# Optimization experiments

Hardware: AMD Instinct MI355X
Metric: run time of the kernel (lower is better)

## Reference

```python
import jax, jax.numpy as jnp
import numpy as np

# Geometry / discretization constants (mirrors WaveCell.__init__)
NX, NY = 192, 192
DT = 1e-3
CMAX = 1.0
H = DT * CMAX * np.sqrt(2.0) * 1.01  # auto-set h as in __init__ (satisfies CFL)
SRC_X, SRC_Y = 96, 32  # point source grid location


def _laplacian(y, inv_h2):
    # y: [B, Nx, Ny]; 5-point stencil with zero padding (conv2d padding=1)
    p = jnp.pad(y, ((0, 0), (1, 1), (1, 1)))
    return inv_h2 * (p[:, :-2, 1:-1] + p[:, 2:, 1:-1]
                     + p[:, 1:-1, :-2] + p[:, 1:-1, 2:] - 4.0 * y)


def setup_inputs() -> dict:
    key = jax.random.key(0)
    k1, k2, k3 = jax.random.split(key, 3)
    B, T = 4, 256
    x = jax.random.normal(k1, (B, T, 1), dtype=jnp.float32)
    # per-cell wave speed in [0,1) so cmax <= 1 (CFL-safe)
    c = jax.random.uniform(k2, (NX, NY), dtype=jnp.float32)
    # boundary absorber damping coefficient
    b = jax.random.uniform(k3, (NX, NY), dtype=jnp.float32)
    return {"x": x, "c": c, "b": b}


def reference(x, c, b):
    B, T = x.shape[0], x.shape[1]
    inv_h2 = 1.0 / (H * H)
    inv_dt2 = 1.0 / (DT * DT)
    a_inv = 1.0 / (inv_dt2 + 0.5 * b / DT)   # [Nx, Ny]
    coef2 = inv_dt2 - 0.5 * b / DT           # [Nx, Ny]
    c2 = c * c

    x_seq = jnp.transpose(x[..., 0], (1, 0))  # [T, B]

    def step(carry, xt):
        y1, y2 = carry  # fields one and two steps ago
        y = a_inv * (2.0 * inv_dt2 * y1 - coef2 * y2 + c2 * _laplacian(y1, inv_h2))
        y = y.at[:, SRC_X, SRC_Y].add(xt)  # point source injection
        return (y, y1), y

    y0 = jnp.zeros((B, NX, NY), dtype=x.dtype)
    _, ys = jax.lax.scan(step, (y0, y0), x_seq)  # ys: [T, B, Nx, Ny]
    return jnp.transpose(ys, (1, 0, 2, 3))       # [B, T, Nx, Ny]
```

## Files before the change

### kernel.cpp

```cpp
#include <hip/hip_runtime.h>


#define NXg 192
#define NYg 192
#define BATCH 4
#define TSTEPS 256
#define CELLS (NXg * NYg)

#define TS 24
#define KSTEP 16
#define EXT 56
#define LROWS (EXT + 2)
#define LPITCH 68
#define LSZ (LROWS * LPITCH)
#define NTHREADS 448

#define SRC_X 96
#define SRC_Y 32

__global__ __launch_bounds__(NTHREADS) void wave_tile_kernel(
    const float* __restrict__ cgp, const float* __restrict__ bgp,
    const float* __restrict__ x, float* __restrict__ out, int t0) {
  __shared__ float buf0[LSZ];
  __shared__ float buf1[LSZ];

  const int tid = threadIdx.x;
  const int lr = tid >> 3;
  const int lg = tid & 7;
  const int bcol = blockIdx.x;
  const int brow = blockIdx.y;
  const int bb = blockIdx.z;
  const int r0 = brow * TS - KSTEP;
  const int c0 = bcol * TS - KSTEP;
  const int obase = bb * TSTEPS * CELLS;
  const float inv_h2 = (float)(1.0 / (2.0 * 1.01 * 1.01 * 1.0e-3 * 1.0e-3));

  const int gr = r0 + lr;
  const int gc = c0 + 8 * lg;
  const bool id = (lg < 7) && (gr >= 0) && (gr < NXg) && (gc >= 0) && (gc < NYg);
  const bool til = (lr >= KSTEP) && (lr < KSTEP + TS) && (lg >= 2) && (lg < 5);
  const bool hs = (SRC_X >= r0) && (SRC_X < r0 + EXT) &&
                  (SRC_Y >= c0) && (SRC_Y < c0 + EXT);
  const int gofs = id ? (gr * NYg + gc) : 0;

  const float4 z4 = make_float4(0.f, 0.f, 0.f, 0.f);

  float4 cv0 = z4, cv1 = z4, bv0 = z4, bv1 = z4;
  float4 yc0 = z4, yc1 = z4, yp0 = z4, yp1 = z4;
  if (id) {
    cv0 = *(const float4*)(cgp + gofs);
    cv1 = *(const float4*)(cgp + gofs + 4);
    bv0 = *(const float4*)(bgp + gofs);
    bv1 = *(const float4*)(bgp + gofs + 4);
    if (t0 > 0) {
      yc0 = *(const float4*)(out + obase + (t0 - 1) * CELLS + gofs);
      yc1 = *(const float4*)(out + obase + (t0 - 1) * CELLS + gofs + 4);
      yp0 = *(const float4*)(out + obase + (t0 - 2) * CELLS + gofs);
      yp1 = *(const float4*)(out + obase + (t0 - 2) * CELLS + gofs + 4);
    }
  }
  float xs[KSTEP];
  {
    const float4* xp = (const float4*)(x + bb * TSTEPS + t0);
    float4 a0 = xp[0], a1 = xp[1], a2 = xp[2], a3 = xp[3];
    xs[0] = a0.x; xs[1] = a0.y; xs[2] = a0.z; xs[3] = a0.w;
    xs[4] = a1.x; xs[5] = a1.y; xs[6] = a1.z; xs[7] = a1.w;
    xs[8] = a2.x; xs[9] = a2.y; xs[10] = a2.z; xs[11] = a2.w;
    xs[12] = a3.x; xs[13] = a3.y; xs[14] = a3.z; xs[15] = a3.w;
  }

  float4 Dc0 = z4, Dc1 = z4, Ey0 = z4, Ey1 = z4, G0 = z4, G1 = z4;
  float4 sm0 = z4, sm1 = z4;
  if (id) {
    float ai;
    ai = 1.0f / (1.0e6f + 500.0f * bv0.x);
    Dc0.x = 2.0e6f * ai; Ey0.x = (1.0e6f - 500.0f * bv0.x) * ai;
    G0.x = (cv0.x * cv0.x) * inv_h2 * ai;
    ai = 1.0f / (1.0e6f + 500.0f * bv0.y);
    Dc0.y = 2.0e6f * ai; Ey0.y = (1.0e6f - 500.0f * bv0.y) * ai;
    G0.y = (cv0.y * cv0.y) * inv_h2 * ai;
    ai = 1.0f / (1.0e6f + 500.0f * bv0.z);
    Dc0.z = 2.0e6f * ai; Ey0.z = (1.0e6f - 500.0f * bv0.z) * ai;
    G0.z = (cv0.z * cv0.z) * inv_h2 * ai;
    ai = 1.0f / (1.0e6f + 500.0f * bv0.w);
    Dc0.w = 2.0e6f * ai; Ey0.w = (1.0e6f - 500.0f * bv0.w) * ai;
    G0.w = (cv0.w * cv0.w) * inv_h2 * ai;
    ai = 1.0f / (1.0e6f + 500.0f * bv1.x);
    Dc1.x = 2.0e6f * ai; Ey1.x = (1.0e6f - 500.0f * bv1.x) * ai;
    G1.x = (cv1.x * cv1.x) * inv_h2 * ai;
    ai = 1.0f / (1.0e6f + 500.0f * bv1.y);
    Dc1.y = 2.0e6f * ai; Ey1.y = (1.0e6f - 500.0f * bv1.y) * ai;
    G1.y = (cv1.y * cv1.y) * inv_h2 * ai;
    ai = 1.0f / (1.0e6f + 500.0f * bv1.z);
    Dc1.z = 2.0e6f * ai; Ey1.z = (1.0e6f - 500.0f * bv1.z) * ai;
    G1.z = (cv1.z * cv1.z) * inv_h2 * ai;
    ai = 1.0f / (1.0e6f + 500.0f * bv1.w);
    Dc1.w = 2.0e6f * ai; Ey1.w = (1.0e6f - 500.0f * bv1.w) * ai;
    G1.w = (cv1.w * cv1.w) * inv_h2 * ai;
    if (gr == SRC_X) {
      sm0.x = (gc + 0 == SRC_Y) ? 1.0f : 0.0f;
      sm0.y = (gc + 1 == SRC_Y) ? 1.0f : 0.0f;
      sm0.z = (gc + 2 == SRC_Y) ? 1.0f : 0.0f;
      sm0.w = (gc + 3 == SRC_Y) ? 1.0f : 0.0f;
      sm1.x = (gc + 4 == SRC_Y) ? 1.0f : 0.0f;
      sm1.y = (gc + 5 == SRC_Y) ? 1.0f : 0.0f;
      sm1.z = (gc + 6 == SRC_Y) ? 1.0f : 0.0f;
      sm1.w = (gc + 7 == SRC_Y) ? 1.0f : 0.0f;
    }
  }

  const int lo = (lr + 1) * LPITCH + 4 + 8 * lg;
  *(float4*)&buf0[lo] = yc0;
  *(float4*)&buf0[lo + 4] = yc1;
  __syncthreads();

  float* ping = buf0;
  float* pong = buf1;

  float4 pv0 = z4, pv1 = z4;
  float* pop = out;

#define CELL(dst, up_, dn_, lf_, rt_, D_, E_, Gc_, y_, p_)              \
  {                                                                     \
    float s_ = fmaf(-4.0f, y_, (up_ + dn_) + (lf_ + rt_));              \
    dst = fmaf(Gc_, s_, fmaf(-E_, p_, D_ * y_));                        \
  }

#pragma unroll
  for (int j = 0; j < KSTEP; ++j) {
    const float xt = xs[j];
    float* op = out + obase + (t0 + j) * CELLS;

    if (j > 0 && til) {
      *(float4*)(pop + gofs) = pv0;
      *(float4*)(pop + gofs + 4) = pv1;
    }

    const bool alive = (lr >= j + 1) && (lr <= 54 - j);
    if (alive) {
      float lqw = __shfl_up(yc1.w, 1);
      lqw = (lg == 0) ? 0.0f : lqw;
      float rqx = __shfl_down(yc0.x, 1);
      rqx = (lg == 7) ? 0.0f : rqx;

      float4 up0 = *(float4*)&ping[lo - LPITCH];
      float4 up1 = *(float4*)&ping[lo - LPITCH + 4];
      float4 dn0 = *(float4*)&ping[lo + LPITCH];
      float4 dn1 = *(float4*)&ping[lo + LPITCH + 4];

      float4 val0, val1;
      CELL(val0.x, up0.x, dn0.x, lqw,    yc0.y, Dc0.x, Ey0.x, G0.x, yc0.x, yp0.x);
      CELL(val0.y, up0.y, dn0.y, yc0.x,  yc0.z, Dc0.y, Ey0.y, G0.y, yc0.y, yp0.y);
      CELL(val0.z, up0.z, dn0.z, yc0.y,  yc0.w, Dc0.z, Ey0.z, G0.z, yc0.z, yp0.z);
      CELL(val0.w, up0.w, dn0.w, yc0.z,  yc1.x, Dc0.w, Ey0.w, G0.w, yc0.w, yp0.w);
      CELL(val1.x, up1.x, dn1.x, yc0.w,  yc1.y, Dc1.x, Ey1.x, G1.x, yc1.x, yp1.x);
      CELL(val1.y, up1.y, dn1.y, yc1.x,  yc1.z, Dc1.y, Ey1.y, G1.y, yc1.y, yp1.y);
      CELL(val1.z, up1.z, dn1.z, yc1.y,  yc1.w, Dc1.z, Ey1.z, G1.z, yc1.z, yp1.z);
      CELL(val1.w, up1.w, dn1.w, yc1.z,  rqx,   Dc1.w, Ey1.w, G1.w, yc1.w, yp1.w);

      if (hs) {
        val0.x = fmaf(sm0.x, xt, val0.x);
        val0.y = fmaf(sm0.y, xt, val0.y);
        val0.z = fmaf(sm0.z, xt, val0.z);
        val0.w = fmaf(sm0.w, xt, val0.w);
        val1.x = fmaf(sm1.x, xt, val1.x);
        val1.y = fmaf(sm1.y, xt, val1.y);
        val1.z = fmaf(sm1.z, xt, val1.z);
        val1.w = fmaf(sm1.w, xt, val1.w);
      }

      yp0 = yc0; yp1 = yc1;
      yc0 = val0; yc1 = val1;

      *(float4*)&pong[lo] = val0;
      *(float4*)&pong[lo + 4] = val1;

      pv0 = val0; pv1 = val1;
    }
    pop = op;

    __syncthreads();
    float* tmp = ping; ping = pong; pong = tmp;
  }
#undef CELL

  if (til) {
    *(float4*)(pop + gofs) = pv0;
    *(float4*)(pop + gofs + 4) = pv1;
  }
}

extern "C" void kernel_launch(void* const* d_in, const int* in_sizes, int n_in,
                              void* d_out, int out_size, void* d_ws,
                              size_t ws_size, hipStream_t stream) {
  const float* x = (const float*)d_in[0];
  const float* c = (const float*)d_in[1];
  const float* b = (const float*)d_in[2];
  float* out = (float*)d_out;

  dim3 grid(NXg / TS, NYg / TS, BATCH);
  for (int t0 = 0; t0 < TSTEPS; t0 += KSTEP) {
    wave_tile_kernel<<<grid, NTHREADS, 0, stream>>>(c, b, x, out, t0);
  }
}
```

Before: 324.2 us.

## Run each tile in a single wavefront with register slots, dropping block barriers

Each tile is now handled by one 64-lane wavefront in which every thread owns 7 row slots, replacing the 448-thread block. This removes __syncthreads between time steps, relying on a single wave plus an lgkmcnt wait for LDS ordering. The per-step live-row trimming is dropped, so every slot computes every step, and the update is refactored to y + E*(y-p) + G*lap to save a multiply. The costs are far fewer waves in flight (256 single-wave blocks), heavy register pressure, and serialised work per wave, which may hurt latency hiding.

```diff
diff --git a/kernel.cpp b/kernel.cpp
--- a/kernel.cpp
+++ b/kernel.cpp
@@ -10,23 +10,30 @@
 #define TS 24
 #define KSTEP 16
 #define EXT 56
-#define LROWS (EXT + 2)
+#define LROWS 58
 #define LPITCH 68
 #define LSZ (LROWS * LPITCH)
-#define NTHREADS 448
+#define NSLOT 7
 
 #define SRC_X 96
 #define SRC_Y 32
 
-__global__ __launch_bounds__(NTHREADS) void wave_tile_kernel(
+#define CELL(dst, up_, dn_, lf_, rt_, E_, G_, y_, p_)                  \
+  {                                                                    \
+    float s_ = fmaf(-4.0f, y_, (up_ + dn_) + (lf_ + rt_));             \
+    dst = fmaf(G_, s_, fmaf(E_, (y_ - p_), y_));                       \
+  }
+
+__global__ __launch_bounds__(64, 1) void wave_kernel(
     const float* __restrict__ cgp, const float* __restrict__ bgp,
     const float* __restrict__ x, float* __restrict__ out, int t0) {
   __shared__ float buf0[LSZ];
   __shared__ float buf1[LSZ];
-
-  const int tid = threadIdx.x;
-  const int lr = tid >> 3;
-  const int lg = tid & 7;
+  __shared__ float xsL[KSTEP];
+
+  const int lane = threadIdx.x;
+  const int rs = lane >> 3;
+  const int lg = lane & 7;
   const int bcol = blockIdx.x;
   const int brow = blockIdx.y;
   const int bb = blockIdx.z;
@@ -35,158 +42,151 @@
   const int obase = bb * TSTEPS * CELLS;
   const float inv_h2 = (float)(1.0 / (2.0 * 1.01 * 1.01 * 1.0e-3 * 1.0e-3));
 
-  const int gr = r0 + lr;
   const int gc = c0 + 8 * lg;
-  const bool id = (lg < 7) && (gr >= 0) && (gr < NXg) && (gc >= 0) && (gc < NYg);
-  const bool til = (lr >= KSTEP) && (lr < KSTEP + TS) && (lg >= 2) && (lg < 5);
+  const bool colOK = (lg < 7) && (gc >= 0) && (gc < NYg);
   const bool hs = (SRC_X >= r0) && (SRC_X < r0 + EXT) &&
                   (SRC_Y >= c0) && (SRC_Y < c0 + EXT);
-  const int gofs = id ? (gr * NYg + gc) : 0;
 
   const float4 z4 = make_float4(0.f, 0.f, 0.f, 0.f);
 
-  float4 cv0 = z4, cv1 = z4, bv0 = z4, bv1 = z4;
-  float4 yc0 = z4, yc1 = z4, yp0 = z4, yp1 = z4;
-  if (id) {
-    cv0 = *(const float4*)(cgp + gofs);
-    cv1 = *(const float4*)(cgp + gofs + 4);
-    bv0 = *(const float4*)(bgp + gofs);
-    bv1 = *(const float4*)(bgp + gofs + 4);
-    if (t0 > 0) {
-      yc0 = *(const float4*)(out + obase + (t0 - 1) * CELLS + gofs);
-      yc1 = *(const float4*)(out + obase + (t0 - 1) * CELLS + gofs + 4);
-      yp0 = *(const float4*)(out + obase + (t0 - 2) * CELLS + gofs);
-      yp1 = *(const float4*)(out + obase + (t0 - 2) * CELLS + gofs + 4);
+  float4 smc0 = z4, smc1 = z4;
+  if (colOK) {
+    smc0.x = (gc + 0 == SRC_Y) ? 1.0f : 0.0f;
+    smc0.y = (gc + 1 == SRC_Y) ? 1.0f : 0.0f;
+    smc0.z = (gc + 2 == SRC_Y) ? 1.0f : 0.0f;
+    smc0.w = (gc + 3 == SRC_Y) ? 1.0f : 0.0f;
+    smc1.x = (gc + 4 == SRC_Y) ? 1.0f : 0.0f;
+    smc1.y = (gc + 5 == SRC_Y) ? 1.0f : 0.0f;
+    smc1.z = (gc + 6 == SRC_Y) ? 1.0f : 0.0f;
+    smc1.w = (gc + 7 == SRC_Y) ? 1.0f : 0.0f;
+  }
+
+  int offs[NSLOT];
+  int gofs[NSLOT];
+  bool idv[NSLOT];
+  bool tils[NSLOT];
+  float fs[NSLOT];
+  float4 E[NSLOT][2], G[NSLOT][2];
+  float4 yc[NSLOT][2], yp[NSLOT][2];
+
+#pragma unroll
+  for (int s = 0; s < NSLOT; ++s) {
+    const int lr = rs + 8 * s;
+    const int gr = r0 + lr;
+    const bool idr = colOK && (gr >= 0) && (gr < NXg);
+    idv[s] = idr;
+    gofs[s] = idr ? (gr * NYg + gc) : 0;
+    offs[s] = (lr + 1) * LPITCH + 4 + 8 * lg;
+    tils[s] = (s >= 2) && (s <= 4) && (lg >= 2) && (lg < 5);
+    fs[s] = (gr == SRC_X) ? 1.0f : 0.0f;
+    E[s][0] = z4; E[s][1] = z4; G[s][0] = z4; G[s][1] = z4;
+    yc[s][0] = z4; yc[s][1] = z4; yp[s][0] = z4; yp[s][1] = z4;
+    if (idr) {
+      float4 cv0 = *(const float4*)(cgp + gofs[s]);
+      float4 cv1 = *(const float4*)(cgp + gofs[s] + 4);
+      float4 bv0 = *(const float4*)(bgp + gofs[s]);
+      float4 bv1 = *(const float4*)(bgp + gofs[s] + 4);
+      float ai;
+      ai = 1.0f / (1.0e6f + 500.0f * bv0.x);
+      E[s][0].x = (1.0e6f - 500.0f * bv0.x) * ai; G[s][0].x = cv0.x * cv0.x * inv_h2 * ai;
+      ai = 1.0f / (1.0e6f + 500.0f * bv0.y);
+      E[s][0].y = (1.0e6f - 500.0f * bv0.y) * ai; G[s][0].y = cv0.y * cv0.y * inv_h2 * ai;
+      ai = 1.0f / (1.0e6f + 500.0f * bv0.z);
+      E[s][0].z = (1.0e6f - 500.0f * bv0.z) * ai; G[s][0].z = cv0.z * cv0.z * inv_h2 * ai;
+      ai = 1.0f / (1.0e6f + 500.0f * bv0.w);
+      E[s][0].w = (1.0e6f - 500.0f * bv0.w) * ai; G[s][0].w = cv0.w * cv0.w * inv_h2 * ai;
+      ai = 1.0f / (1.0e6f + 500.0f * bv1.x);
+      E[s][1].x = (1.0e6f - 500.0f * bv1.x) * ai; G[s][1].x = cv1.x * cv1.x * inv_h2 * ai;
+      ai = 1.0f / (1.0e6f + 500.0f * bv1.y);
+      E[s][1].y = (1.0e6f - 500.0f * bv1.y) * ai; G[s][1].y = cv1.y * cv1.y * inv_h2 * ai;
+      ai = 1.0f / (1.0e6f + 500.0f * bv1.z);
+      E[s][1].z = (1.0e6f - 500.0f * bv1.z) * ai; G[s][1].z = cv1.z * cv1.z * inv_h2 * ai;
+      ai = 1.0f / (1.0e6f + 500.0f * bv1.w);
+      E[s][1].w = (1.0e6f - 500.0f * bv1.w) * ai; G[s][1].w = cv1.w * cv1.w * inv_h2 * ai;
+      if (t0 > 0) {
+        const float* o1 = out + obase + (t0 - 1) * CELLS;
+        const float* o2 = out + obase + (t0 - 2) * CELLS;
+        yc[s][0] = *(const float4*)(o1 + gofs[s]);
+        yc[s][1] = *(const float4*)(o1 + gofs[s] + 4);
+        yp[s][0] = *(const float4*)(o2 + gofs[s]);
+        yp[s][1] = *(const float4*)(o2 + gofs[s] + 4);
+      }
     }
   }
-  float xs[KSTEP];
-  {
-    const float4* xp = (const float4*)(x + bb * TSTEPS + t0);
-    float4 a0 = xp[0], a1 = xp[1], a2 = xp[2], a3 = xp[3];
-    xs[0] = a0.x; xs[1] = a0.y; xs[2] = a0.z; xs[3] = a0.w;
-    xs[4] = a1.x; xs[5] = a1.y; xs[6] = a1.z; xs[7] = a1.w;
-    xs[8] = a2.x; xs[9] = a2.y; xs[10] = a2.z; xs[11] = a2.w;
-    xs[12] = a3.x; xs[13] = a3.y; xs[14] = a3.z; xs[15] = a3.w;
-  }
-
-  float4 Dc0 = z4, Dc1 = z4, Ey0 = z4, Ey1 = z4, G0 = z4, G1 = z4;
-  float4 sm0 = z4, sm1 = z4;
-  if (id) {
-    float ai;
-    ai = 1.0f / (1.0e6f + 500.0f * bv0.x);
-    Dc0.x = 2.0e6f * ai; Ey0.x = (1.0e6f - 500.0f * bv0.x) * ai;
-    G0.x = (cv0.x * cv0.x) * inv_h2 * ai;
-    ai = 1.0f / (1.0e6f + 500.0f * bv0.y);
-    Dc0.y = 2.0e6f * ai; Ey0.y = (1.0e6f - 500.0f * bv0.y) * ai;
-    G0.y = (cv0.y * cv0.y) * inv_h2 * ai;
-    ai = 1.0f / (1.0e6f + 500.0f * bv0.z);
-    Dc0.z = 2.0e6f * ai; Ey0.z = (1.0e6f - 500.0f * bv0.z) * ai;
-    G0.z = (cv0.z * cv0.z) * inv_h2 * ai;
-    ai = 1.0f / (1.0e6f + 500.0f * bv0.w);
-    Dc0.w = 2.0e6f * ai; Ey0.w = (1.0e6f - 500.0f * bv0.w) * ai;
-    G0.w = (cv0.w * cv0.w) * inv_h2 * ai;
-    ai = 1.0f / (1.0e6f + 500.0f * bv1.x);
-    Dc1.x = 2.0e6f * ai; Ey1.x = (1.0e6f - 500.0f * bv1.x) * ai;
-    G1.x = (cv1.x * cv1.x) * inv_h2 * ai;
-    ai = 1.0f / (1.0e6f + 500.0f * bv1.y);
-    Dc1.y = 2.0e6f * ai; Ey1.y = (1.0e6f - 500.0f * bv1.y) * ai;
-    G1.y = (cv1.y * cv1.y) * inv_h2 * ai;
-    ai = 1.0f / (1.0e6f + 500.0f * bv1.z);
-    Dc1.z = 2.0e6f * ai; Ey1.z = (1.0e6f - 500.0f * bv1.z) * ai;
-    G1.z = (cv1.z * cv1.z) * inv_h2 * ai;
-    ai = 1.0f / (1.0e6f + 500.0f * bv1.w);
-    Dc1.w = 2.0e6f * ai; Ey1.w = (1.0e6f - 500.0f * bv1.w) * ai;
-    G1.w = (cv1.w * cv1.w) * inv_h2 * ai;
-    if (gr == SRC_X) {
-      sm0.x = (gc + 0 == SRC_Y) ? 1.0f : 0.0f;
-      sm0.y = (gc + 1 == SRC_Y) ? 1.0f : 0.0f;
-      sm0.z = (gc + 2 == SRC_Y) ? 1.0f : 0.0f;
-      sm0.w = (gc + 3 == SRC_Y) ? 1.0f : 0.0f;
-      sm1.x = (gc + 4 == SRC_Y) ? 1.0f : 0.0f;
-      sm1.y = (gc + 5 == SRC_Y) ? 1.0f : 0.0f;
-      sm1.z = (gc + 6 == SRC_Y) ? 1.0f : 0.0f;
-      sm1.w = (gc + 7 == SRC_Y) ? 1.0f : 0.0f;
-    }
-  }
-
-  const int lo = (lr + 1) * LPITCH + 4 + 8 * lg;
-  *(float4*)&buf0[lo] = yc0;
-  *(float4*)&buf0[lo + 4] = yc1;
-  __syncthreads();
+
+  if (lane < 4) {
+    float4 a = ((const float4*)(x + bb * TSTEPS + t0))[lane];
+    *(float4*)&xsL[4 * lane] = a;
+  }
+
+  for (int i = lane; i < 2 * LPITCH; i += 64) {
+    const int row = (i < LPITCH) ? 0 : (LROWS - 1);
+    const int cidx = i % LPITCH;
+    buf0[row * LPITCH + cidx] = 0.f;
+    buf1[row * LPITCH + cidx] = 0.f;
+  }
+
+#pragma unroll
+  for (int s = 0; s < NSLOT; ++s) {
+    *(float4*)&buf0[offs[s]] = yc[s][0];
+    *(float4*)&buf0[offs[s] + 4] = yc[s][1];
+  }
 
   float* ping = buf0;
   float* pong = buf1;
 
-  float4 pv0 = z4, pv1 = z4;
-  float* pop = out;
-
-#define CELL(dst, up_, dn_, lf_, rt_, D_, E_, Gc_, y_, p_)              \
-  {                                                                     \
-    float s_ = fmaf(-4.0f, y_, (up_ + dn_) + (lf_ + rt_));              \
-    dst = fmaf(Gc_, s_, fmaf(-E_, p_, D_ * y_));                        \
-  }
+#pragma clang loop unroll(disable)
+  for (int j = 0; j < KSTEP; ++j) {
+    asm volatile("s_waitcnt lgkmcnt(0)" ::: "memory");
+    const float xt = xsL[j];
+    float* op = out + obase + (t0 + j) * CELLS;
 
 #pragma unroll
-  for (int j = 0; j < KSTEP; ++j) {
-    const float xt = xs[j];
-    float* op = out + obase + (t0 + j) * CELLS;
-
-    if (j > 0 && til) {
-      *(float4*)(pop + gofs) = pv0;
-      *(float4*)(pop + gofs + 4) = pv1;
+    for (int s = 0; s < NSLOT; ++s) {
+      float4 up0 = *(float4*)&ping[offs[s] - LPITCH];
+      float4 up1 = *(float4*)&ping[offs[s] - LPITCH + 4];
+      float4 dn0 = *(float4*)&ping[offs[s] + LPITCH];
+      float4 dn1 = *(float4*)&ping[offs[s] + LPITCH + 4];
+
+      float lq = __shfl_up(yc[s][1].w, 1);
+      lq = (lg == 0) ? 0.0f : lq;
+      float rq = __shfl_down(yc[s][0].x, 1);
+      rq = (lg == 7) ? 0.0f : rq;
+
+      float4 v0, v1;
+      CELL(v0.x, up0.x, dn0.x, lq,         yc[s][0].y, E[s][0].x, G[s][0].x, yc[s][0].x, yp[s][0].x);
+      CELL(v0.y, up0.y, dn0.y, yc[s][0].x, yc[s][0].z, E[s][0].y, G[s][0].y, yc[s][0].y, yp[s][0].y);
+      CELL(v0.z, up0.z, dn0.z, yc[s][0].y, yc[s][0].w, E[s][0].z, G[s][0].z, yc[s][0].z, yp[s][0].z);
+      CELL(v0.w, up0.w, dn0.w, yc[s][0].z, yc[s][1].x, E[s][0].w, G[s][0].w, yc[s][0].w, yp[s][0].w);
+      CELL(v1.x, up1.x, dn1.x, yc[s][0].w, yc[s][1].y, E[s][1].x, G[s][1].x, yc[s][1].x, yp[s][1].x);
+      CELL(v1.y, up1.y, dn1.y, yc[s][1].x, yc[s][1].z, E[s][1].y, G[s][1].y, yc[s][1].y, yp[s][1].y);
+      CELL(v1.z, up1.z, dn1.z, yc[s][1].y, yc[s][1].w, E[s][1].z, G[s][1].z, yc[s][1].z, yp[s][1].z);
+      CELL(v1.w, up1.w, dn1.w, yc[s][1].z, rq,         E[s][1].w, G[s][1].w, yc[s][1].w, yp[s][1].w);
+
+      if (hs) {
+        const float fx = fs[s] * xt;
+        v0.x = fmaf(smc0.x, fx, v0.x);
+        v0.y = fmaf(smc0.y, fx, v0.y);
+        v0.z = fmaf(smc0.z, fx, v0.z);
+        v0.w = fmaf(smc0.w, fx, v0.w);
+        v1.x = fmaf(smc1.x, fx, v1.x);
+        v1.y = fmaf(smc1.y, fx, v1.y);
+        v1.z = fmaf(smc1.z, fx, v1.z);
+        v1.w = fmaf(smc1.w, fx, v1.w);
+      }
+
+      if (tils[s]) {
+        *(float4*)(op + gofs[s]) = v0;
+        *(float4*)(op + gofs[s] + 4) = v1;
+      }
+
+      *(float4*)&pong[offs[s]] = v0;
+      *(float4*)&pong[offs[s] + 4] = v1;
+      yp[s][0] = yc[s][0]; yp[s][1] = yc[s][1];
+      yc[s][0] = v0;       yc[s][1] = v1;
     }
 
-    const bool alive = (lr >= j + 1) && (lr <= 54 - j);
-    if (alive) {
-      float lqw = __shfl_up(yc1.w, 1);
-      lqw = (lg == 0) ? 0.0f : lqw;
-      float rqx = __shfl_down(yc0.x, 1);
-      rqx = (lg == 7) ? 0.0f : rqx;
-
-      float4 up0 = *(float4*)&ping[lo - LPITCH];
-      float4 up1 = *(float4*)&ping[lo - LPITCH + 4];
-      float4 dn0 = *(float4*)&ping[lo + LPITCH];
-      float4 dn1 = *(float4*)&ping[lo + LPITCH + 4];
-
-      float4 val0, val1;
-      CELL(val0.x, up0.x, dn0.x, lqw,    yc0.y, Dc0.x, Ey0.x, G0.x, yc0.x, yp0.x);
-      CELL(val0.y, up0.y, dn0.y, yc0.x,  yc0.z, Dc0.y, Ey0.y, G0.y, yc0.y, yp0.y);
-      CELL(val0.z, up0.z, dn0.z, yc0.y,  yc0.w, Dc0.z, Ey0.z, G0.z, yc0.z, yp0.z);
-      CELL(val0.w, up0.w, dn0.w, yc0.z,  yc1.x, Dc0.w, Ey0.w, G0.w, yc0.w, yp0.w);
-      CELL(val1.x, up1.x, dn1.x, yc0.w,  yc1.y, Dc1.x, Ey1.x, G1.x, yc1.x, yp1.x);
-      CELL(val1.y, up1.y, dn1.y, yc1.x,  yc1.z, Dc1.y, Ey1.y, G1.y, yc1.y, yp1.y);
-      CELL(val1.z, up1.z, dn1.z, yc1.y,  yc1.w, Dc1.z, Ey1.z, G1.z, yc1.z, yp1.z);
-      CELL(val1.w, up1.w, dn1.w, yc1.z,  rqx,   Dc1.w, Ey1.w, G1.w, yc1.w, yp1.w);
-
-      if (hs) {
-        val0.x = fmaf(sm0.x, xt, val0.x);
-        val0.y = fmaf(sm0.y, xt, val0.y);
-        val0.z = fmaf(sm0.z, xt, val0.z);
-        val0.w = fmaf(sm0.w, xt, val0.w);
-        val1.x = fmaf(sm1.x, xt, val1.x);
-        val1.y = fmaf(sm1.y, xt, val1.y);
-        val1.z = fmaf(sm1.z, xt, val1.z);
-        val1.w = fmaf(sm1.w, xt, val1.w);
-      }
-
-      yp0 = yc0; yp1 = yc1;
-      yc0 = val0; yc1 = val1;
-
-      *(float4*)&pong[lo] = val0;
-      *(float4*)&pong[lo + 4] = val1;
-
-      pv0 = val0; pv1 = val1;
-    }
-    pop = op;
-
-    __syncthreads();
-    float* tmp = ping; ping = pong; pong = tmp;
-  }
-#undef CELL
-
-  if (til) {
-    *(float4*)(pop + gofs) = pv0;
-    *(float4*)(pop + gofs + 4) = pv1;
+    float* t_ = ping; ping = pong; pong = t_;
   }
 }
 
@@ -200,6 +200,6 @@
 
   dim3 grid(NXg / TS, NYg / TS, BATCH);
   for (int t0 = 0; t0 < TSTEPS; t0 += KSTEP) {
-    wave_tile_kernel<<<grid, NTHREADS, 0, stream>>>(c, b, x, out, t0);
+    wave_kernel<<<grid, 64, 0, stream>>>(c, b, x, out, t0);
   }
 }
```

After: 777.2 us. 140% more time.
